# Kernel tuning notes

Measured on AMD Instinct MI355X. Metric: run time of the kernel, lower is better.

Reference implementation:

```python
import jax, jax.numpy as jnp
import numpy as np

N_TASKS = 8
D_MODEL = 1024
HIDDEN = 1024
N_CLASSES = 100
BATCH = 8192


def setup_inputs() -> dict:
    key = jax.random.key(0)
    ks = jax.random.split(key, 6)
    s1 = 1.0 / np.sqrt(D_MODEL)
    s2 = 1.0 / np.sqrt(HIDDEN)
    return {
        "x": jax.random.normal(ks[0], (BATCH, D_MODEL), dtype=jnp.float32),
        "task_id": jax.random.randint(ks[1], (BATCH,), 0, N_TASKS),
        "W1": jax.random.uniform(ks[2], (N_TASKS, D_MODEL, HIDDEN), jnp.float32, -s1, s1),
        "b1": jax.random.uniform(ks[3], (N_TASKS, HIDDEN), jnp.float32, -s1, s1),
        "W2": jax.random.uniform(ks[4], (N_TASKS, HIDDEN, N_CLASSES), jnp.float32, -s2, s2),
        "b2": jax.random.uniform(ks[5], (N_TASKS, N_CLASSES), jnp.float32, -s2, s2),
    }


def reference(x, task_id, W1, b1, W2, b2):
    # Per-task 2-layer MLP heads; dropout is identity (inference).
    # Compute all heads batched, then select each row's head via one-hot.
    h = jax.nn.relu(jnp.einsum("bd,tdh->tbh", x, W1) + b1[:, None, :])  # [T,B,H]
    logits = jnp.einsum("tbh,thc->tbc", h, W2) + b2[:, None, :]          # [T,B,C]
    onehot = jax.nn.one_hot(task_id, W1.shape[0], dtype=x.dtype)          # [B,T]
    return jnp.einsum("tbc,bt->bc", logits, onehot)                      # [B,C]
```

## Files before the change

### kernel.cpp

```cpp
#include <hip/hip_runtime.h>
#include <hip/hip_bf16.h>
#include <stdint.h>

#define T_TASKS 8
#define DM      1024
#define HID     1024
#define NC      100
#define NCP     128
#define BATCH   8192
#define MPAD    9216

typedef __bf16 bf16x8 __attribute__((ext_vector_type(8)));
typedef float  f32x4  __attribute__((ext_vector_type(4)));
typedef unsigned int u32;
#define GAS __attribute__((address_space(1)))
#define LAS __attribute__((address_space(3)))

__device__ __forceinline__ unsigned short f2bf(float f) {
  __hip_bfloat16 h = __float2bfloat16(f);
  return __builtin_bit_cast(unsigned short, h);
}

__device__ __forceinline__ float bf2f(unsigned short u) {
  const u32 v = ((u32)u) << 16;
  return __builtin_bit_cast(float, v);
}

#define SORT_BLKS 32
#define W1_BLKS (T_TASKS * 16 * 16)
#define W2_BLKS (16 * T_TASKS)
__global__ void sortpre_k(const int* __restrict__ task_id,
                          const float* __restrict__ W1,
                          unsigned short* __restrict__ W1T,
                          const float* __restrict__ W2,
                          unsigned short* __restrict__ W2F,
                          int* __restrict__ perm, int* __restrict__ starts) {
  __shared__ __align__(16) unsigned short tile[128 * 72];
  __shared__ int sAux[25];
  const int bid = blockIdx.x;
  const int tid = threadIdx.x;

  if (bid < SORT_BLKS) {
    int* hist = (int*)tile;
    int* tot  = sAux;
    int* prev = sAux + 8;
    int* sst  = sAux + 16;
#pragma unroll
    for (int t = 0; t < T_TASKS; ++t) hist[tid * 8 + t] = 0;
    __syncthreads();
    const int cbase = tid * 32;
    for (int i = 0; i < 32; ++i) {
      const int t = task_id[cbase + i];
      hist[tid * 8 + t] += 1;
    }
    __syncthreads();
    if (tid < T_TASKS) {
      int s = 0;
      for (int r = 0; r < 256; ++r) s += hist[r * 8 + tid];
      tot[tid] = s;
    } else if (tid < 2 * T_TASKS) {
      const int t = tid - T_TASKS;
      const int lim = bid * 8;
      int s = 0;
      for (int r = 0; r < lim; ++r) s += hist[r * 8 + t];
      prev[t] = s;
    }
    __syncthreads();
    if (tid == 0) {
      int off = 0;
      for (int t = 0; t < T_TASKS; ++t) { sst[t] = off; off += (tot[t] + 127) & ~127; }
      sst[T_TASKS] = off;
    }
    if (tid < T_TASKS) hist[tid] = 0;
    __syncthreads();
    const int r = bid * 256 + tid;
    const int t = task_id[r];
    const int slot = atomicAdd(&hist[t], 1);
    perm[sst[t] + prev[t] + slot] = r;
    if (tid < 32) {
      const int g = bid * 32 + tid;
      int acc = 0, pos = -1;
#pragma unroll
      for (int t2 = 0; t2 < T_TASKS; ++t2) {
        const int pc = sst[t2 + 1] - sst[t2] - tot[t2];
        if (pos < 0 && g < acc + pc) pos = sst[t2] + tot[t2] + (g - acc);
        acc += pc;
      }
      if (pos < 0) pos = sst[T_TASKS] + (g - acc);
      perm[pos] = -1;
    }
    if (bid == 0 && tid <= T_TASKS) starts[tid] = sst[tid];
    return;
  }

  if (bid < SORT_BLKS + W1_BLKS) {
    const int b  = bid - SORT_BLKS;
    const int t  = b >> 8;
    const int rem = b & 255;
    const int d0 = (rem >> 4) * 64;
    const int h0 = (rem & 15) * 64;
    const float* src = W1 + (size_t)t * DM * HID;
    unsigned short* dst = W1T + (size_t)t * HID * DM;
#pragma unroll
    for (int i = 0; i < 4; ++i) {
      const int idx = tid + 256 * i;
      const int d  = idx >> 4;
      const int hc = (idx & 15) * 4;
      const float4 f = *(const float4*)(src + (size_t)(d0 + d) * HID + h0 + hc);
      tile[(hc + 0) * 65 + d] = f2bf(f.x);
      tile[(hc + 1) * 65 + d] = f2bf(f.y);
      tile[(hc + 2) * 65 + d] = f2bf(f.z);
      tile[(hc + 3) * 65 + d] = f2bf(f.w);
    }
    __syncthreads();
#pragma unroll
    for (int i = 0; i < 2; ++i) {
      const int idx = tid + 256 * i;
      const int lh  = idx >> 3;
      const int ldc = idx & 7;
      union { uint4 v; unsigned short s[8]; } o;
#pragma unroll
      for (int q = 0; q < 8; ++q) o.s[q] = tile[lh * 65 + ldc * 8 + q];
      *(uint4*)(dst + (size_t)(h0 + lh) * DM + d0 + ldc * 8) = o.v;
    }
    return;
  }

  {
    const int b  = bid - (SORT_BLKS + W1_BLKS);
    const int t  = b >> 4;
    const int h0 = (b & 15) * 64;
    const float* src = W2 + (size_t)t * HID * NC;
#pragma unroll
    for (int i = 0; i < 36; ++i) tile[tid + 256 * i] = 0;
    __syncthreads();
#pragma unroll
    for (int i = 0; i < 32; ++i) {
      const int idx = tid + 256 * i;
      const int row = idx >> 7, col = idx & 127;
      if (col < NC)
        tile[col * 72 + row] = f2bf(src[(size_t)(h0 + row) * NC + col]);
    }
    __syncthreads();
    const int w = tid >> 6, lane = tid & 63;
    const int lr = lane & 15, quad = lane >> 4;
#pragma unroll
    for (int e = 0; e < 4; ++e) {
      const int fi = w * 4 + e;
      const int ci = fi >> 1, kcl = fi & 1;
      const uint4 v = *(const uint4*)&tile[(ci * 16 + lr) * 72 + kcl * 32 + quad * 8];
      unsigned short* dstp =
          W2F + (((size_t)t * 8 + ci) * 32 + (h0 >> 5) + kcl) * 512 + lane * 8;
      *(uint4*)dstp = v;
    }
  }
}

__global__ void gather_k(const float* __restrict__ x,
                         const int* __restrict__ perm,
                         unsigned short* __restrict__ XP) {
  const int bid = blockIdx.x;
  const int tid = threadIdx.x;
  const int r = perm[bid];
  const int c = tid * 4;
  ushort4 v;
  if (r >= 0) {
    const float4 f = *(const float4*)(x + (size_t)r * DM + c);
    v.x = f2bf(f.x); v.y = f2bf(f.y); v.z = f2bf(f.z); v.w = f2bf(f.w);
  } else {
    v.x = 0; v.y = 0; v.z = 0; v.w = 0;
  }
  *(ushort4*)(XP + (size_t)bid * DM + c) = v;
}

__global__ __launch_bounds__(256, 3) void gemm_fused4(
    const unsigned short* __restrict__ XP,
    const unsigned short* __restrict__ W1T,
    const unsigned short* __restrict__ W2F,
    const float* __restrict__ b1,
    const int* __restrict__ starts,
    unsigned short* __restrict__ Lp)
{
  __shared__ __align__(16) unsigned short lds[18432];
  unsigned short* As = lds;
  unsigned short* Bs = lds + 8192;
  unsigned short* hS = lds;

  const int tid = threadIdx.x;

  const int L   = blockIdx.y * gridDim.x + blockIdx.x;
  const int xcd = L & 7;
  const int idx = L >> 3;
  const int bx  = xcd * 9 + (idx % 9);
  const int by  = idx / 9;

  const int p0  = bx * 128;
  const int n0  = by * 128;

  if (p0 >= starts[T_TASKS]) return;

  int task = 0;
#pragma unroll
  for (int t = 1; t < T_TASKS; ++t)
    if (p0 >= starts[t]) task = t;

  const int wave = tid >> 6;
  const int lane = tid & 63;
  const int wm   = (wave >> 1) * 64;
  const int wn   = (wave & 1) * 64;
  const int lr   = lane & 15;
  const int quad = lane >> 4;

  const int crow = tid >> 3;
  const int kc   = (tid & 7) ^ (crow & 7);
  const unsigned short* pA[4];
  const unsigned short* pB[4];
  const unsigned short* Bg = W1T + ((size_t)task * HID + n0) * 1024;
#pragma unroll
  for (int i = 0; i < 4; ++i) {
    const int row = crow + 32 * i;
    pA[i] = XP + (size_t)(p0 + row) * 1024 + kc * 8;
    pB[i] = Bg + (size_t)row * 1024 + kc * 8;
  }

  f32x4 acc[4][4];
#pragma unroll
  for (int i = 0; i < 4; ++i)
#pragma unroll
    for (int j = 0; j < 4; ++j) acc[i][j] = (f32x4){0.f, 0.f, 0.f, 0.f};

  const int sw0 = quad ^ (lr & 7);
  const int sw1 = (4 + quad) ^ (lr & 7);

  for (int k0 = 0; k0 < 1024; k0 += 64) {
#pragma unroll
    for (int i = 0; i < 4; ++i) {
      __builtin_amdgcn_global_load_lds((const GAS u32*)(pA[i] + k0),
                                       (LAS u32*)&As[(tid + 256 * i) * 8], 16, 0, 0);
      __builtin_amdgcn_global_load_lds((const GAS u32*)(pB[i] + k0),
                                       (LAS u32*)&Bs[(tid + 256 * i) * 8], 16, 0, 0);
    }
    __syncthreads();
    {
      bf16x8 a[4], b[4];
#pragma unroll
      for (int i = 0; i < 4; ++i)
        a[i] = *(const bf16x8*)&As[((wm + i * 16 + lr) * 8 + sw0) * 8];
#pragma unroll
      for (int j = 0; j < 4; ++j)
        b[j] = *(const bf16x8*)&Bs[((wn + j * 16 + lr) * 8 + sw0) * 8];
#pragma unroll
      for (int i = 0; i < 4; ++i)
#pragma unroll
        for (int j = 0; j < 4; ++j)
          acc[i][j] = __builtin_amdgcn_mfma_f32_16x16x32_bf16(a[i], b[j], acc[i][j], 0, 0, 0);
#pragma unroll
      for (int i = 0; i < 4; ++i)
        a[i] = *(const bf16x8*)&As[((wm + i * 16 + lr) * 8 + sw1) * 8];
#pragma unroll
      for (int j = 0; j < 4; ++j)
        b[j] = *(const bf16x8*)&Bs[((wn + j * 16 + lr) * 8 + sw1) * 8];
#pragma unroll
      for (int i = 0; i < 4; ++i)
#pragma unroll
        for (int j = 0; j < 4; ++j)
          acc[i][j] = __builtin_amdgcn_mfma_f32_16x16x32_bf16(a[i], b[j], acc[i][j], 0, 0, 0);
    }
    __syncthreads();
  }

  float b1v[4];
#pragma unroll
  for (int ni = 0; ni < 4; ++ni)
    b1v[ni] = b1[task * HID + n0 + wn + ni * 16 + lr];
#pragma unroll
  for (int mi = 0; mi < 4; ++mi)
#pragma unroll
    for (int r = 0; r < 4; ++r) {
      const int row = wm + mi * 16 + quad * 4 + r;
#pragma unroll
      for (int ni = 0; ni < 4; ++ni) {
        float v = acc[mi][ni][r] + b1v[ni];
        v = v > 0.f ? v : 0.f;
        hS[row * 136 + wn + ni * 16 + lr] = f2bf(v);
      }
    }
  __syncthreads();

  const int cbase = (wave & 1) * 4;
  const unsigned short* pW2 =
      W2F + (((size_t)task * 8 + cbase) * 32 + by * 4) * 512 + lane * 8;

  f32x4 acc2[4][4];
#pragma unroll
  for (int mi = 0; mi < 4; ++mi)
#pragma unroll
    for (int ci = 0; ci < 4; ++ci) acc2[mi][ci] = (f32x4){0.f, 0.f, 0.f, 0.f};

#pragma unroll
  for (int e = 0; e < 4; ++e) {
    bf16x8 w2p[4], a2[4];
#pragma unroll
    for (int ci = 0; ci < 4; ++ci)
      w2p[ci] = *(const bf16x8*)(pW2 + ((size_t)ci * 32 + e) * 512);
#pragma unroll
    for (int mi = 0; mi < 4; ++mi)
      a2[mi] = *(const bf16x8*)&hS[(wm + mi * 16 + lr) * 136 + e * 32 + quad * 8];
#pragma unroll
    for (int mi = 0; mi < 4; ++mi)
#pragma unroll
      for (int ci = 0; ci < 4; ++ci)
        acc2[mi][ci] = __builtin_amdgcn_mfma_f32_16x16x32_bf16(
            a2[mi], w2p[ci], acc2[mi][ci], 0, 0, 0);
  }

  unsigned short* lp = Lp + ((size_t)by * MPAD + p0) * NCP;
#pragma unroll
  for (int mi = 0; mi < 4; ++mi)
#pragma unroll
    for (int r = 0; r < 4; ++r) {
      const int row = wm + mi * 16 + quad * 4 + r;
#pragma unroll
      for (int ci = 0; ci < 4; ++ci)
        lp[row * NCP + wn + ci * 16 + lr] = f2bf(acc2[mi][ci][r]);
    }
}

__global__ void reduce_k(const unsigned short* __restrict__ Lp,
                         const int* __restrict__ perm,
                         const int* __restrict__ task_id,
                         const float* __restrict__ b2,
                         float* __restrict__ Out) {
  const int gid = blockIdx.x * 256 + threadIdx.x;
  const int row = gid >> 5;
  const int c4  = (gid & 31) * 4;
  if (c4 >= NC) return;
  const int og = perm[row];
  if (og < 0) return;
  float s0 = 0.f, s1 = 0.f, s2 = 0.f, s3 = 0.f;
#pragma unroll
  for (int sp = 0; sp < 8; ++sp) {
    const ushort4 v = *(const ushort4*)(Lp + ((size_t)sp * MPAD + row) * NCP + c4);
    s0 += bf2f(v.x); s1 += bf2f(v.y); s2 += bf2f(v.z); s3 += bf2f(v.w);
  }
  const int task = task_id[og];
  const float4 bb = *(const float4*)(b2 + (size_t)task * NC + c4);
  float4 o;
  o.x = s0 + bb.x; o.y = s1 + bb.y; o.z = s2 + bb.z; o.w = s3 + bb.w;
  *(float4*)(Out + (size_t)og * NC + c4) = o;
}

extern "C" void kernel_launch(void* const* d_in, const int* in_sizes, int n_in,
                              void* d_out, int out_size, void* d_ws, size_t ws_size,
                              hipStream_t stream) {
  const float* x       = (const float*)d_in[0];
  const int*   task_id = (const int*)d_in[1];
  const float* W1      = (const float*)d_in[2];
  const float* b1      = (const float*)d_in[3];
  const float* W2      = (const float*)d_in[4];
  const float* b2      = (const float*)d_in[5];
  float* out = (float*)d_out;

  char* ws = (char*)d_ws;
  int* perm   = (int*)(ws + 0);
  int* starts = (int*)(ws + 37888);
  unsigned short* XP  = (unsigned short*)(ws + 65536);
  unsigned short* W1T = (unsigned short*)(ws + 18939904);
  unsigned short* W2F = (unsigned short*)(ws + 35717120);
  unsigned short* Lp  = (unsigned short*)(ws + 37814272);

  sortpre_k<<<SORT_BLKS + W1_BLKS + W2_BLKS, 256, 0, stream>>>(
      task_id, W1, W1T, W2, W2F, perm, starts);
  gather_k<<<MPAD, 256, 0, stream>>>(x, perm, XP);
  gemm_fused4<<<dim3(MPAD / 128, HID / 128), 256, 0, stream>>>(
      XP, W1T, W2F, b1, starts, Lp);
  reduce_k<<<MPAD * 32 / 256, 256, 0, stream>>>(Lp, perm, task_id, b2, out);
}
```

Measured before the change: 149.4 us.

## Fuse split-hidden reduction into GEMM epilogue via fp32 atomics, drop reduce kernel

Result: slower. 174.3 us (+16.6%).

```diff
diff --git a/kernel.cpp b/kernel.cpp
--- a/kernel.cpp
+++ b/kernel.cpp
@@ -29,11 +29,14 @@
 #define SORT_BLKS 32
 #define W1_BLKS (T_TASKS * 16 * 16)
 #define W2_BLKS (16 * T_TASKS)
+#define OUT_BLKS (BATCH / 8)
 __global__ void sortpre_k(const int* __restrict__ task_id,
                           const float* __restrict__ W1,
                           unsigned short* __restrict__ W1T,
                           const float* __restrict__ W2,
                           unsigned short* __restrict__ W2F,
+                          const float* __restrict__ b2,
+                          float* __restrict__ Out,
                           int* __restrict__ perm, int* __restrict__ starts) {
   __shared__ __align__(16) unsigned short tile[128 * 72];
   __shared__ int sAux[25];
@@ -126,7 +129,7 @@
     return;
   }
 
-  {
+  if (bid < SORT_BLKS + W1_BLKS + W2_BLKS) {
     const int b  = bid - (SORT_BLKS + W1_BLKS);
     const int t  = b >> 4;
     const int h0 = (b & 15) * 64;
@@ -152,6 +155,19 @@
       unsigned short* dstp =
           W2F + (((size_t)t * 8 + ci) * 32 + (h0 >> 5) + kcl) * 512 + lane * 8;
       *(uint4*)dstp = v;
+    }
+    return;
+  }
+
+  {
+    const int b = bid - (SORT_BLKS + W1_BLKS + W2_BLKS);
+    const int row = b * 8 + (tid >> 5);
+    const int c = (tid & 31) * 4;
+    if (c < NC) {
+      const int t = task_id[row];
+      const float* src = b2 + (size_t)t * NC + c;
+      float* dst = Out + (size_t)row * NC + c;
+      dst[0] = src[0]; dst[1] = src[1]; dst[2] = src[2]; dst[3] = src[3];
     }
   }
 }
@@ -179,9 +195,11 @@
     const unsigned short* __restrict__ W2F,
     const float* __restrict__ b1,
     const int* __restrict__ starts,
-    unsigned short* __restrict__ Lp)
+    const int* __restrict__ perm,
+    float* __restrict__ Out)
 {
   __shared__ __align__(16) unsigned short lds[18432];
+  __shared__ int ogS[128];
   unsigned short* As = lds;
   unsigned short* Bs = lds + 8192;
   unsigned short* hS = lds;
@@ -198,6 +216,8 @@
   const int n0  = by * 128;
 
   if (p0 >= starts[T_TASKS]) return;
+
+  if (tid < 128) ogS[tid] = perm[p0 + tid];
 
   int task = 0;
 #pragma unroll
@@ -314,40 +334,21 @@
             a2[mi], w2p[ci], acc2[mi][ci], 0, 0, 0);
   }
 
-  unsigned short* lp = Lp + ((size_t)by * MPAD + p0) * NCP;
 #pragma unroll
   for (int mi = 0; mi < 4; ++mi)
 #pragma unroll
     for (int r = 0; r < 4; ++r) {
       const int row = wm + mi * 16 + quad * 4 + r;
-#pragma unroll
-      for (int ci = 0; ci < 4; ++ci)
-        lp[row * NCP + wn + ci * 16 + lr] = f2bf(acc2[mi][ci][r]);
-    }
-}
-
-__global__ void reduce_k(const unsigned short* __restrict__ Lp,
-                         const int* __restrict__ perm,
-                         const int* __restrict__ task_id,
-                         const float* __restrict__ b2,
-                         float* __restrict__ Out) {
-  const int gid = blockIdx.x * 256 + threadIdx.x;
-  const int row = gid >> 5;
-  const int c4  = (gid & 31) * 4;
-  if (c4 >= NC) return;
-  const int og = perm[row];
-  if (og < 0) return;
-  float s0 = 0.f, s1 = 0.f, s2 = 0.f, s3 = 0.f;
-#pragma unroll
-  for (int sp = 0; sp < 8; ++sp) {
-    const ushort4 v = *(const ushort4*)(Lp + ((size_t)sp * MPAD + row) * NCP + c4);
-    s0 += bf2f(v.x); s1 += bf2f(v.y); s2 += bf2f(v.z); s3 += bf2f(v.w);
-  }
-  const int task = task_id[og];
-  const float4 bb = *(const float4*)(b2 + (size_t)task * NC + c4);
-  float4 o;
-  o.x = s0 + bb.x; o.y = s1 + bb.y; o.z = s2 + bb.z; o.w = s3 + bb.w;
-  *(float4*)(Out + (size_t)og * NC + c4) = o;
+      const int og  = ogS[row];
+      if (og >= 0) {
+        float* orow = Out + (size_t)og * NC;
+#pragma unroll
+        for (int ci = 0; ci < 4; ++ci) {
+          const int col = wn + ci * 16 + lr;
+          if (col < NC) atomicAdd(orow + col, acc2[mi][ci][r]);
+        }
+      }
+    }
 }
 
 extern "C" void kernel_launch(void* const* d_in, const int* in_sizes, int n_in,
@@ -367,12 +368,10 @@
   unsigned short* XP  = (unsigned short*)(ws + 65536);
   unsigned short* W1T = (unsigned short*)(ws + 18939904);
   unsigned short* W2F = (unsigned short*)(ws + 35717120);
-  unsigned short* Lp  = (unsigned short*)(ws + 37814272);
-
-  sortpre_k<<<SORT_BLKS + W1_BLKS + W2_BLKS, 256, 0, stream>>>(
-      task_id, W1, W1T, W2, W2F, perm, starts);
+
+  sortpre_k<<<SORT_BLKS + W1_BLKS + W2_BLKS + OUT_BLKS, 256, 0, stream>>>(
+      task_id, W1, W1T, W2, W2F, b2, out, perm, starts);
   gather_k<<<MPAD, 256, 0, stream>>>(x, perm, XP);
   gemm_fused4<<<dim3(MPAD / 128, HID / 128), 256, 0, stream>>>(
-      XP, W1T, W2F, b1, starts, Lp);
-  reduce_k<<<MPAD * 32 / 256, 256, 0, stream>>>(Lp, perm, task_id, b2, out);
-}
+      XP, W1T, W2F, b1, starts, perm, out);
+}
```
